# Optimization experiments

Measured on AMD Instinct MI355X. Metric: run time of the kernel, lower is better.

Reference implementation:

```python
import jax, jax.numpy as jnp
import numpy as np

B = 65536      # batch size
L = 1024       # nlabels (relation vocabulary)
X = 32         # max number of correct labels per sample
TOL = 1e-6


def setup_inputs() -> dict:
    key = jax.random.key(0)
    k1, k2, k3 = jax.random.split(key, 3)
    # predictions: positive values (the original sums raw values then logs them)
    prd = jax.random.uniform(k1, (B, L), dtype=jnp.float32)
    labels = jax.random.randint(k2, (B, X), 0, L, dtype=jnp.int32)
    # last column: number of valid labels, in [1, X]
    n = jax.random.randint(k3, (B, 1), 1, X + 1, dtype=jnp.int32)
    tgt = jnp.concatenate([labels, n], axis=1)  # [B, X+1]
    return {"prd": prd, "tgt": tgt}


def reference(prd, tgt):
    # tgt[:, :-1] = padded label indices, tgt[:, -1] = count of valid labels
    labels = tgt[:, :-1]                                   # [B, X]
    n = tgt[:, -1]                                         # [B]
    mask = jnp.arange(labels.shape[1]) < n[:, None]        # [B, X] ragged mask
    gathered = jnp.take_along_axis(prd, labels, axis=1)    # [B, X]
    s = jnp.where(mask, gathered, jnp.zeros((), prd.dtype)).sum(axis=1)  # [B]
    loss = -jnp.log(s + TOL)                               # [B]
    # reduction=True: average over batch
    return loss.sum() / prd.shape[0]
```

## Files before the change

kernel.cpp:

```cpp
#include <hip/hip_runtime.h>
#include <math.h>


#define NROWS   65536
#define LCOLS   1024
#define TGT_LD  33
#define TOLV    1e-6f
#define INV_B   (1.0f / 65536.0f)

__global__ __launch_bounds__(256)
void mlce_kernel(const float* __restrict__ prd,
                 const int*   __restrict__ tgt,
                 float*       __restrict__ out)
{
    const int tid = blockIdx.x * blockDim.x + threadIdx.x;
    const int row = tid >> 5;
    const int j   = tid & 31;

    float loss = 0.0f;
    if (row < NROWS) {
        const int base = row * TGT_LD;
        const int n    = tgt[base + 32];
        float v = 0.0f;
        if (j < n) {
            const int lab = tgt[base + j];
            v = prd[row * LCOLS + lab];
        }
        #pragma unroll
        for (int off = 16; off > 0; off >>= 1)
            v += __shfl_xor(v, off, 32);
        if (j == 0)
            loss = -logf(v + TOLV);
    }

    #pragma unroll
    for (int off = 32; off > 0; off >>= 1)
        loss += __shfl_xor(loss, off, 64);

    __shared__ float smem[4];
    const int wid  = threadIdx.x >> 6;
    const int lane = threadIdx.x & 63;
    if (lane == 0) smem[wid] = loss;
    __syncthreads();
    if (threadIdx.x == 0) {
        const float t = smem[0] + smem[1] + smem[2] + smem[3];
        atomicAdd(out, t * INV_B);
    }
}

extern "C" void kernel_launch(void* const* d_in, const int* in_sizes, int n_in,
                              void* d_out, int out_size, void* d_ws, size_t ws_size,
                              hipStream_t stream)
{
    const float* prd = (const float*)d_in[0];
    const int*   tgt = (const int*)d_in[1];
    float*       out = (float*)d_out;

    hipMemsetAsync(out, 0, sizeof(float), stream);

    const int threads = 256;
    const int total   = NROWS * 32;
    const int blocks  = total / threads;
    mlce_kernel<<<blocks, threads, 0, stream>>>(prd, tgt, out);
}
```

Measured before the change: 395.7 us.

## Stream whole prd rows into LDS and gather labels from shared memory

Each wave now loads its entire 1024-float prediction row with coalesced float4 reads into shared memory, then gathers the labelled entries from LDS instead of doing scattered global loads. One wave handles one row, and the label/count loads are merged into a single per-lane read. This swaps random 4-byte gathers for full contiguous reads of the row, which move far more bytes (4 KB per row versus up to 32 scattered floats). It also adds a 16 KB LDS footprint per block, which limits occupancy.

```diff
diff --git a/kernel.cpp b/kernel.cpp
--- a/kernel.cpp
+++ b/kernel.cpp
@@ -7,43 +7,47 @@
 #define TGT_LD  33
 #define TOLV    1e-6f
 #define INV_B   (1.0f / 65536.0f)
+#define WAVES_PER_BLOCK 4
 
 __global__ __launch_bounds__(256)
 void mlce_kernel(const float* __restrict__ prd,
                  const int*   __restrict__ tgt,
                  float*       __restrict__ out)
 {
-    const int tid = blockIdx.x * blockDim.x + threadIdx.x;
-    const int row = tid >> 5;
-    const int j   = tid & 31;
+    __shared__ float rowbuf[WAVES_PER_BLOCK][LCOLS];
+    __shared__ float partial[WAVES_PER_BLOCK];
 
-    float loss = 0.0f;
-    if (row < NROWS) {
-        const int base = row * TGT_LD;
-        const int n    = tgt[base + 32];
-        float v = 0.0f;
-        if (j < n) {
-            const int lab = tgt[base + j];
-            v = prd[row * LCOLS + lab];
-        }
-        #pragma unroll
-        for (int off = 16; off > 0; off >>= 1)
-            v += __shfl_xor(v, off, 32);
-        if (j == 0)
-            loss = -logf(v + TOLV);
-    }
+    const int w    = threadIdx.x >> 6;
+    const int lane = threadIdx.x & 63;
+    const int row  = blockIdx.x * WAVES_PER_BLOCK + w;
+
+    const float4* __restrict__ src = (const float4*)(prd + row * LCOLS);
+    float4* dst = (float4*)rowbuf[w];
+    #pragma unroll
+    for (int i = 0; i < 4; ++i)
+        dst[lane + i * 64] = src[lane + i * 64];
+
+    const int base = row * TGT_LD;
+    int lab = 0;
+    if (lane < TGT_LD) lab = tgt[base + lane];
+    const int n = __shfl(lab, 32, 64);
+
+    __syncthreads();
+
+    float v = 0.0f;
+    if (lane < 32 && lane < n)
+        v = rowbuf[w][lab];
 
     #pragma unroll
     for (int off = 32; off > 0; off >>= 1)
-        loss += __shfl_xor(loss, off, 64);
+        v += __shfl_xor(v, off, 64);
 
-    __shared__ float smem[4];
-    const int wid  = threadIdx.x >> 6;
-    const int lane = threadIdx.x & 63;
-    if (lane == 0) smem[wid] = loss;
+    if (lane == 0)
+        partial[w] = -logf(v + TOLV);
     __syncthreads();
+
     if (threadIdx.x == 0) {
-        const float t = smem[0] + smem[1] + smem[2] + smem[3];
+        const float t = partial[0] + partial[1] + partial[2] + partial[3];
         atomicAdd(out, t * INV_B);
     }
 }
@@ -58,8 +62,6 @@
 
     hipMemsetAsync(out, 0, sizeof(float), stream);
 
-    const int threads = 256;
-    const int total   = NROWS * 32;
-    const int blocks  = total / threads;
-    mlce_kernel<<<blocks, threads, 0, stream>>>(prd, tgt, out);
+    const int blocks = NROWS / WAVES_PER_BLOCK;
+    mlce_kernel<<<blocks, 256, 0, stream>>>(prd, tgt, out);
 }
```

Result: slower. 482.8 us (+22.0%).
